# Kernel optimization log

Measured on AMD Instinct MI355X. Metric: run time of the kernel, lower is better.

## Reference

```python
import jax, jax.numpy as jnp
import numpy as np

DELTA_PULL = 0.5
DELTA_PUSH = 1.5
EPS = 1e-6


def setup_inputs() -> dict:
    key = jax.random.key(0)
    k1, k2 = jax.random.split(key)
    B, C, H, W, K = 4, 16, 512, 512, 16
    embedding_maps = jax.random.normal(k1, (B, C, H, W), dtype=jnp.float32)
    instance_masks = jax.random.randint(k2, (B, K, H, W), 0, 2, dtype=jnp.int32)
    return {"embedding_maps": embedding_maps, "instance_masks": instance_masks}


def reference(embedding_maps, instance_masks):
    emb = embedding_maps                      # [B, C, H, W]
    m = (instance_masks > 0).astype(emb.dtype)  # [B, K, H, W]
    K = m.shape[1]

    # per-instance masked segment reductions over all H*W pixels
    counts = m.sum((-1, -2))                                   # [B, K]
    sums = jnp.einsum('bchw,bkhw->bkc', emb, m)                # [B, K, C]
    sq_sums = jnp.einsum('bchw,bkhw->bkc', emb * emb, m)       # [B, K, C]

    valid = counts > 0                                          # [B, K]
    safe_counts = jnp.maximum(counts, 1.0)
    means = sums / safe_counts[..., None]                       # [B, K, C] exact fg mean

    # sum over fg pixels of ||e - mean||^2 = sq_sum - 2*mean.sum + n*mean^2
    pull_k = (sq_sums - 2.0 * means * sums + counts[..., None] * means * means).sum(-1)
    pull_k = jnp.where(valid, pull_k / (counts + EPS), 0.0)     # [B, K]

    M = valid.sum(-1).astype(emb.dtype)                         # [B] num valid instances
    pull_b = pull_k.sum(-1) / jnp.maximum(M, 1.0)               # [B]

    # pairwise push between valid instance means (i < j)
    diff = means[:, :, None, :] - means[:, None, :, :]          # [B, K, K, C]
    dist = jnp.sqrt((diff * diff).sum(-1) + 1e-12)              # [B, K, K]
    iu = jnp.arange(K)
    pair = valid[:, :, None] & valid[:, None, :] & (iu[:, None] < iu[None, :])
    push_terms = jnp.where(pair, jnp.maximum(DELTA_PUSH - dist, 0.0) ** 2, 0.0)
    npairs = M * (M - 1.0) / 2.0
    push_b = jnp.where(M > 1.0, push_terms.sum((-1, -2)) / jnp.maximum(npairs, 1.0), 0.0)

    return (DELTA_PULL * pull_b + push_b).mean()
```

## Files before the change

### kernel.cpp

```cpp
#include <hip/hip_runtime.h>

#define BB 4
#define CC 16
#define KK 16
#define HWP (512 * 512)
#define TILE 1024
#define NTILES (HWP / TILE)
#define THREADS 256
#define JITERS (TILE / 64)
#define NSLICE 8
#define WSTOT (64 + 1024 + 1024)

typedef float f2 __attribute__((ext_vector_type(2)));

__device__ __forceinline__ float fmaxf_(float a, float b) { return a > b ? a : b; }

__device__ __forceinline__ f2 fma2(float m, f2 ee, f2 acc) {
#if __has_builtin(__builtin_elementwise_fma)
    f2 mm = {m, m};
    return __builtin_elementwise_fma(mm, ee, acc);
#else
    acc.x = fmaf(m, ee.x, acc.x);
    acc.y = fmaf(m, ee.y, acc.y);
    return acc;
#endif
}

__global__ __launch_bounds__(THREADS, 4) void disc_partial_kernel(
    const float* __restrict__ emb, const int* __restrict__ masks,
    float* __restrict__ ws)
{
    __shared__ unsigned short bits[TILE];
    __shared__ int wcnt[4][KK];

    const int tid = threadIdx.x;
    const int b = blockIdx.x / NTILES;
    const int tile = blockIdx.x % NTILES;
    const size_t tile0 = (size_t)tile * TILE;
    float* slice = ws + (size_t)(blockIdx.x & (NSLICE - 1)) * WSTOT;

    const int4* mbase4 = (const int4*)(masks + (size_t)b * KK * HWP + tile0);
    unsigned v0 = 0, v1 = 0, v2 = 0, v3 = 0;
    #pragma unroll
    for (int k = 0; k < KK; ++k) {
        int4 mm = mbase4[(size_t)k * (HWP / 4) + tid];
        v0 |= (mm.x > 0 ? 1u : 0u) << k;
        v1 |= (mm.y > 0 ? 1u : 0u) << k;
        v2 |= (mm.z > 0 ? 1u : 0u) << k;
        v3 |= (mm.w > 0 ? 1u : 0u) << k;
    }
    uint2 packed;
    packed.x = v0 | (v1 << 16);
    packed.y = v2 | (v3 << 16);
    ((uint2*)bits)[tid] = packed;

    const int lane = tid & 63;
    const int wave = tid >> 6;
    int mycnt = 0;
    #pragma unroll
    for (int k = 0; k < KK; ++k) {
        unsigned long long b0 = __ballot((v0 >> k) & 1u);
        unsigned long long b1 = __ballot((v1 >> k) & 1u);
        unsigned long long b2 = __ballot((v2 >> k) & 1u);
        unsigned long long b3 = __ballot((v3 >> k) & 1u);
        if (lane == k) mycnt = __popcll(b0) + __popcll(b1) + __popcll(b2) + __popcll(b3);
    }
    if (lane < KK) wcnt[wave][lane] = mycnt;
    __syncthreads();

    const int c = tid >> 4;
    const int l = tid & 15;
    const float4* e4 = (const float4*)(emb + ((size_t)b * CC + c) * HWP + tile0);
    const ushort4* b4 = (const ushort4*)bits;

    f2 acc[KK];
    #pragma unroll
    for (int k = 0; k < KK; ++k) { acc[k].x = 0.f; acc[k].y = 0.f; }

    #pragma unroll 4
    for (int j = 0; j < JITERS; ++j) {
        float4 e = e4[j * 16 + l];
        ushort4 vv = b4[j * 16 + l];
        const float ex[4] = {e.x, e.y, e.z, e.w};
        const unsigned vx[4] = {vv.x, vv.y, vv.z, vv.w};
        #pragma unroll
        for (int p = 0; p < 4; ++p) {
            float ev = ex[p];
            f2 ee = {ev, ev * ev};
            unsigned v = vx[p];
            #pragma unroll
            for (int k = 0; k < KK; ++k) {
                float fm = (float)((v >> k) & 1u);
                acc[k] = fma2(fm, ee, acc[k]);
            }
        }
    }

    float out_s = 0.f, out_q = 0.f;
    #pragma unroll
    for (int k = 0; k < KK; ++k) {
        float ts = acc[k].x, tq = acc[k].y;
        #pragma unroll
        for (int d = 8; d >= 1; d >>= 1) {
            ts += __shfl_xor(ts, d, 64);
            tq += __shfl_xor(tq, d, 64);
        }
        if (l == k) { out_s = ts; out_q = tq; }
    }
    atomicAdd(&slice[64 + ((size_t)b * KK + l) * CC + c], out_s);
    atomicAdd(&slice[64 + 1024 + ((size_t)b * KK + l) * CC + c], out_q);
    if (tid < KK) {
        float ctot = (float)(wcnt[0][tid] + wcnt[1][tid] + wcnt[2][tid] + wcnt[3][tid]);
        atomicAdd(&slice[b * KK + tid], ctot);
    }
}

__global__ __launch_bounds__(256) void disc_finalize_kernel(
    const float* __restrict__ ws, float* __restrict__ out)
{
    __shared__ float red[WSTOT];
    __shared__ float means[BB][KK][CC];
    __shared__ float partial[BB];
    const int tid = threadIdx.x;

    for (int idx = tid; idx < WSTOT; idx += 256) {
        float t = 0.f;
        #pragma unroll
        for (int s = 0; s < NSLICE; ++s) t += ws[(size_t)s * WSTOT + idx];
        red[idx] = t;
    }
    __syncthreads();

    const float* red_cnt = red;
    const float* red_sum = red + 64;
    const float* red_sq  = red + 64 + 1024;

    const int b = tid >> 6;
    const int lane = tid & 63;

    const float DELTA_PULL = 0.5f;
    const float DELTA_PUSH = 1.5f;
    const float EPS = 1e-6f;

    float cntk = 0.f;
    bool valid = false;
    float pull_k = 0.f;
    if (lane < KK) {
        int k = lane;
        cntk = red_cnt[b * KK + k];
        valid = cntk > 0.f;
        float safe = fmaxf_(cntk, 1.f);
        float acc_sq = 0.f, acc_ss = 0.f;
        #pragma unroll
        for (int c = 0; c < CC; ++c) {
            float sv = red_sum[(b * KK + k) * CC + c];
            means[b][k][c] = sv / safe;
            acc_sq += red_sq[(b * KK + k) * CC + c];
            acc_ss += sv * sv;
        }
        if (valid) pull_k = (acc_sq - acc_ss / cntk) / (cntk + EPS);
    }

    unsigned long long bal = __ballot(lane < KK && valid);
    float M = (float)__popcll(bal);

    float ps = pull_k;
    #pragma unroll
    for (int d = 32; d >= 1; d >>= 1) ps += __shfl_xor(ps, d, 64);
    float pull_b = ps / fmaxf_(M, 1.f);

    __syncthreads();

    float push = 0.f;
    for (int t = lane; t < KK * KK; t += 64) {
        int i = t >> 4, j = t & 15;
        if (i < j && ((bal >> i) & 1ull) && ((bal >> j) & 1ull)) {
            float d2 = 1e-12f;
            #pragma unroll
            for (int c = 0; c < CC; ++c) {
                float df = means[b][i][c] - means[b][j][c];
                d2 = fmaf(df, df, d2);
            }
            float dist = sqrtf(d2);
            float h = fmaxf_(DELTA_PUSH - dist, 0.f);
            push += h * h;
        }
    }
    #pragma unroll
    for (int d = 32; d >= 1; d >>= 1) push += __shfl_xor(push, d, 64);

    if (lane == 0) {
        float npairs = M * (M - 1.f) * 0.5f;
        float push_b = (M > 1.f) ? push / fmaxf_(npairs, 1.f) : 0.f;
        partial[b] = DELTA_PULL * pull_b + push_b;
    }
    __syncthreads();
    if (tid == 0) {
        out[0] = (partial[0] + partial[1] + partial[2] + partial[3]) * 0.25f;
    }
}

extern "C" void kernel_launch(void* const* d_in, const int* in_sizes, int n_in,
                              void* d_out, int out_size, void* d_ws, size_t ws_size,
                              hipStream_t stream) {
    const float* emb = (const float*)d_in[0];
    const int* masks = (const int*)d_in[1];
    float* ws = (float*)d_ws;

    hipMemsetAsync(d_ws, 0, NSLICE * WSTOT * sizeof(float), stream);

    dim3 grid(BB * NTILES);
    disc_partial_kernel<<<grid, THREADS, 0, stream>>>(emb, masks, ws);
    disc_finalize_kernel<<<1, 256, 0, stream>>>(ws, (float*)d_out);
}
```

Baseline: 166.1 us.

## Fuse finalize into partial kernel via last-block counter and halve tile size

Merges the finalize pass into the partial-reduction kernel: each block bumps a global atomic counter after a threadfence, and the last block to finish reads the slice workspaces and computes the loss. This removes one kernel launch and its gap. Tile size is also halved to 512 pixels, which doubles the grid and the number of atomics into the shared slices. Each block now reserves about 9KB more LDS for the finalize buffers, which may reduce occupancy.

New measurement: 442.0 us. 166% more time.

```diff
diff --git a/kernel.cpp b/kernel.cpp
--- a/kernel.cpp
+++ b/kernel.cpp
@@ -4,12 +4,13 @@
 #define CC 16
 #define KK 16
 #define HWP (512 * 512)
-#define TILE 1024
+#define TILE 512
 #define NTILES (HWP / TILE)
 #define THREADS 256
 #define JITERS (TILE / 64)
 #define NSLICE 8
 #define WSTOT (64 + 1024 + 1024)
+#define WS_OFF 16
 
 typedef float f2 __attribute__((ext_vector_type(2)));
 
@@ -26,33 +27,33 @@
 #endif
 }
 
-__global__ __launch_bounds__(THREADS, 4) void disc_partial_kernel(
+__global__ __launch_bounds__(THREADS, 4) void disc_fused_kernel(
     const float* __restrict__ emb, const int* __restrict__ masks,
-    float* __restrict__ ws)
+    float* __restrict__ ws, float* __restrict__ out)
 {
     __shared__ unsigned short bits[TILE];
     __shared__ int wcnt[4][KK];
+    __shared__ int is_last;
+    __shared__ float red[WSTOT];
+    __shared__ float means[BB][KK][CC];
+    __shared__ float partial[BB];
 
     const int tid = threadIdx.x;
     const int b = blockIdx.x / NTILES;
     const int tile = blockIdx.x % NTILES;
     const size_t tile0 = (size_t)tile * TILE;
-    float* slice = ws + (size_t)(blockIdx.x & (NSLICE - 1)) * WSTOT;
-
-    const int4* mbase4 = (const int4*)(masks + (size_t)b * KK * HWP + tile0);
-    unsigned v0 = 0, v1 = 0, v2 = 0, v3 = 0;
+    int* counter = (int*)ws;
+    float* slice = ws + WS_OFF + (size_t)(blockIdx.x & (NSLICE - 1)) * WSTOT;
+
+    const int2* mbase2 = (const int2*)(masks + (size_t)b * KK * HWP + tile0);
+    unsigned v0 = 0, v1 = 0;
     #pragma unroll
     for (int k = 0; k < KK; ++k) {
-        int4 mm = mbase4[(size_t)k * (HWP / 4) + tid];
+        int2 mm = mbase2[(size_t)k * (HWP / 2) + tid];
         v0 |= (mm.x > 0 ? 1u : 0u) << k;
         v1 |= (mm.y > 0 ? 1u : 0u) << k;
-        v2 |= (mm.z > 0 ? 1u : 0u) << k;
-        v3 |= (mm.w > 0 ? 1u : 0u) << k;
-    }
-    uint2 packed;
-    packed.x = v0 | (v1 << 16);
-    packed.y = v2 | (v3 << 16);
-    ((uint2*)bits)[tid] = packed;
+    }
+    ((unsigned*)bits)[tid] = v0 | (v1 << 16);
 
     const int lane = tid & 63;
     const int wave = tid >> 6;
@@ -61,9 +62,7 @@
     for (int k = 0; k < KK; ++k) {
         unsigned long long b0 = __ballot((v0 >> k) & 1u);
         unsigned long long b1 = __ballot((v1 >> k) & 1u);
-        unsigned long long b2 = __ballot((v2 >> k) & 1u);
-        unsigned long long b3 = __ballot((v3 >> k) & 1u);
-        if (lane == k) mycnt = __popcll(b0) + __popcll(b1) + __popcll(b2) + __popcll(b3);
+        if (lane == k) mycnt = __popcll(b0) + __popcll(b1);
     }
     if (lane < KK) wcnt[wave][lane] = mycnt;
     __syncthreads();
@@ -113,20 +112,23 @@
         float ctot = (float)(wcnt[0][tid] + wcnt[1][tid] + wcnt[2][tid] + wcnt[3][tid]);
         atomicAdd(&slice[b * KK + tid], ctot);
     }
-}
-
-__global__ __launch_bounds__(256) void disc_finalize_kernel(
-    const float* __restrict__ ws, float* __restrict__ out)
-{
-    __shared__ float red[WSTOT];
-    __shared__ float means[BB][KK][CC];
-    __shared__ float partial[BB];
-    const int tid = threadIdx.x;
-
-    for (int idx = tid; idx < WSTOT; idx += 256) {
+
+    __threadfence();
+    if (tid == 0) {
+        int d = atomicAdd(counter, 1);
+        is_last = (d == (int)gridDim.x - 1);
+    }
+    __syncthreads();
+    if (!is_last) return;
+    __threadfence();
+
+    const float* wsf = ws + WS_OFF;
+    for (int idx = tid; idx < WSTOT; idx += THREADS) {
         float t = 0.f;
         #pragma unroll
-        for (int s = 0; s < NSLICE; ++s) t += ws[(size_t)s * WSTOT + idx];
+        for (int s = 0; s < NSLICE; ++s)
+            t += __hip_atomic_load(&wsf[(size_t)s * WSTOT + idx],
+                                   __ATOMIC_RELAXED, __HIP_MEMORY_SCOPE_AGENT);
         red[idx] = t;
     }
     __syncthreads();
@@ -135,8 +137,8 @@
     const float* red_sum = red + 64;
     const float* red_sq  = red + 64 + 1024;
 
-    const int b = tid >> 6;
-    const int lane = tid & 63;
+    const int fb = tid >> 6;
+    const int flane = tid & 63;
 
     const float DELTA_PULL = 0.5f;
     const float DELTA_PUSH = 1.5f;
@@ -145,23 +147,23 @@
     float cntk = 0.f;
     bool valid = false;
     float pull_k = 0.f;
-    if (lane < KK) {
-        int k = lane;
-        cntk = red_cnt[b * KK + k];
+    if (flane < KK) {
+        int k = flane;
+        cntk = red_cnt[fb * KK + k];
         valid = cntk > 0.f;
         float safe = fmaxf_(cntk, 1.f);
         float acc_sq = 0.f, acc_ss = 0.f;
         #pragma unroll
-        for (int c = 0; c < CC; ++c) {
-            float sv = red_sum[(b * KK + k) * CC + c];
-            means[b][k][c] = sv / safe;
-            acc_sq += red_sq[(b * KK + k) * CC + c];
+        for (int cc = 0; cc < CC; ++cc) {
+            float sv = red_sum[(fb * KK + k) * CC + cc];
+            means[fb][k][cc] = sv / safe;
+            acc_sq += red_sq[(fb * KK + k) * CC + cc];
             acc_ss += sv * sv;
         }
         if (valid) pull_k = (acc_sq - acc_ss / cntk) / (cntk + EPS);
     }
 
-    unsigned long long bal = __ballot(lane < KK && valid);
+    unsigned long long bal = __ballot(flane < KK && valid);
     float M = (float)__popcll(bal);
 
     float ps = pull_k;
@@ -172,13 +174,13 @@
     __syncthreads();
 
     float push = 0.f;
-    for (int t = lane; t < KK * KK; t += 64) {
+    for (int t = flane; t < KK * KK; t += 64) {
         int i = t >> 4, j = t & 15;
         if (i < j && ((bal >> i) & 1ull) && ((bal >> j) & 1ull)) {
             float d2 = 1e-12f;
             #pragma unroll
-            for (int c = 0; c < CC; ++c) {
-                float df = means[b][i][c] - means[b][j][c];
+            for (int cc = 0; cc < CC; ++cc) {
+                float df = means[fb][i][cc] - means[fb][j][cc];
                 d2 = fmaf(df, df, d2);
             }
             float dist = sqrtf(d2);
@@ -189,10 +191,10 @@
     #pragma unroll
     for (int d = 32; d >= 1; d >>= 1) push += __shfl_xor(push, d, 64);
 
-    if (lane == 0) {
+    if (flane == 0) {
         float npairs = M * (M - 1.f) * 0.5f;
         float push_b = (M > 1.f) ? push / fmaxf_(npairs, 1.f) : 0.f;
-        partial[b] = DELTA_PULL * pull_b + push_b;
+        partial[fb] = DELTA_PULL * pull_b + push_b;
     }
     __syncthreads();
     if (tid == 0) {
@@ -207,9 +209,8 @@
     const int* masks = (const int*)d_in[1];
     float* ws = (float*)d_ws;
 
-    hipMemsetAsync(d_ws, 0, NSLICE * WSTOT * sizeof(float), stream);
+    hipMemsetAsync(d_ws, 0, (WS_OFF + NSLICE * WSTOT) * sizeof(float), stream);
 
     dim3 grid(BB * NTILES);
-    disc_partial_kernel<<<grid, THREADS, 0, stream>>>(emb, masks, ws);
-    disc_finalize_kernel<<<1, 256, 0, stream>>>(ws, (float*)d_out);
+    disc_fused_kernel<<<grid, THREADS, 0, stream>>>(emb, masks, ws, (float*)d_out);
 }
```
